# Optimization experiments

Hardware: AMD Instinct MI355X
Metric: run time of the kernel (lower is better)

## Reference

```python
import jax, jax.numpy as jnp
import numpy as np

HIDDEN = 2048
HEADS = 16
HEAD_DIM = HIDDEN // HEADS

def setup_inputs() -> dict:
    key = jax.random.key(0)
    ks = jax.random.split(key, 9)
    B, S = 1, 4096
    scale = 1.0 / np.sqrt(HIDDEN)
    x = jax.random.normal(ks[0], (B, S, HIDDEN), dtype=jnp.float32)
    Wq = jax.random.normal(ks[1], (HIDDEN, HIDDEN), dtype=jnp.float32) * scale
    Wk = jax.random.normal(ks[2], (HIDDEN, HIDDEN), dtype=jnp.float32) * scale
    Wv = jax.random.normal(ks[3], (HIDDEN, HIDDEN), dtype=jnp.float32) * scale
    Wo = jax.random.normal(ks[4], (HIDDEN, HIDDEN), dtype=jnp.float32) * scale
    bq = jax.random.normal(ks[5], (HIDDEN,), dtype=jnp.float32) * 0.01
    bk = jax.random.normal(ks[6], (HIDDEN,), dtype=jnp.float32) * 0.01
    bv = jax.random.normal(ks[7], (HIDDEN,), dtype=jnp.float32) * 0.01
    bo = jax.random.normal(ks[8], (HIDDEN,), dtype=jnp.float32) * 0.01
    return {"x": x, "Wq": Wq, "bq": bq, "Wk": Wk, "bk": bk, "Wv": Wv, "bv": bv, "Wo": Wo, "bo": bo}

def reference(x, Wq, bq, Wk, bk, Wv, bv, Wo, bo):
    B, S, D = x.shape
    H, Hd = HEADS, HEAD_DIM
    # projections (nn.Linear: x @ W^T + b)
    Q = (x @ Wq.T + bq).reshape(B, S, H, Hd).transpose(0, 2, 1, 3)  # [B,H,S,Hd]
    K = (x @ Wk.T + bk).reshape(B, S, H, Hd).transpose(0, 2, 1, 3)
    V = (x @ Wv.T + bv).reshape(B, S, H, Hd).transpose(0, 2, 1, 3)
    scores = jnp.einsum('bhqd,bhkd->bhqk', Q, K) / jnp.sqrt(jnp.float32(Hd))
    attn = jax.nn.softmax(scores, axis=-1)
    out = jnp.einsum('bhqk,bhkd->bhqd', attn, V)  # [B,H,S,Hd]
    out = out.transpose(0, 2, 1, 3).reshape(B, S, D)
    return out @ Wo.T + bo
```

## Files before the change

### kernel.cpp

```cpp
#include <hip/hip_runtime.h>

#define S_LEN  4096
#define DMODEL 2048
#define NHEADS 16
#define HDIM   128

typedef __bf16 bf16x8 __attribute__((ext_vector_type(8)));
typedef __bf16 bf16x2 __attribute__((ext_vector_type(2)));
typedef float  f32x4  __attribute__((ext_vector_type(4)));

__device__ __forceinline__ unsigned short f2b(float f) {
    unsigned int u = __float_as_uint(f);
    unsigned int r = (u + 0x7fffu + ((u >> 16) & 1u)) >> 16;
    return (unsigned short)r;
}

__device__ __forceinline__ unsigned int pkbf16(float a, float b) {
#if __has_builtin(__builtin_amdgcn_cvt_pk_bf16_f32)
    bf16x2 t = __builtin_amdgcn_cvt_pk_bf16_f32(a, b);
    return *(unsigned int*)&t;
#else
    return (unsigned int)f2b(a) | ((unsigned int)f2b(b) << 16);
#endif
}

__device__ __forceinline__ f32x4 mfma16(bf16x8 a, bf16x8 b, f32x4 c) {
    return __builtin_amdgcn_mfma_f32_16x16x32_bf16(a, b, c, 0, 0, 0);
}

__device__ __forceinline__ void ldg2lds16(const void* g, void* l) {
    __builtin_amdgcn_global_load_lds(
        (__attribute__((address_space(1))) void*)(void*)g,
        (__attribute__((address_space(3))) void*)l, 16, 0, 0);
}

__global__ __launch_bounds__(256) void cvt_bf16(
    const float* __restrict__ src, unsigned short* __restrict__ dst, int n4)
{
    int i = blockIdx.x * blockDim.x + threadIdx.x;
    if (i < n4) {
        float4 v = ((const float4*)src)[i];
        uint2 h;
        h.x = pkbf16(v.x, v.y); h.y = pkbf16(v.z, v.w);
        ((uint2*)dst)[i] = h;
    }
}

__global__ __launch_bounds__(256) void cvt_bf16_w4(
    const float* __restrict__ w0, const float* __restrict__ w1,
    const float* __restrict__ w2, const float* __restrict__ w3,
    unsigned short* __restrict__ d0, unsigned short* __restrict__ d1,
    unsigned short* __restrict__ d2, unsigned short* __restrict__ d3)
{
    const int z = blockIdx.y;
    const float* src = (z == 0) ? w0 : (z == 1) ? w1 : (z == 2) ? w2 : w3;
    unsigned short* dst = (z == 0) ? d0 : (z == 1) ? d1 : (z == 2) ? d2 : d3;
    int i = blockIdx.x * blockDim.x + threadIdx.x;
    float4 v = ((const float4*)src)[i];
    uint2 h;
    h.x = pkbf16(v.x, v.y); h.y = pkbf16(v.z, v.w);
    ((uint2*)dst)[i] = h;
}

__global__ __launch_bounds__(256, 2) void gemm_qkv(
    const unsigned short* __restrict__ xb,
    const unsigned short* __restrict__ Wqb, const float* __restrict__ bq,
    const unsigned short* __restrict__ Wkb, const float* __restrict__ bk,
    const unsigned short* __restrict__ Wvb, const float* __restrict__ bv,
    unsigned short* __restrict__ Qb, unsigned short* __restrict__ Kb,
    unsigned short* __restrict__ Vb)
{
    const int z = blockIdx.z;
    const unsigned short* B = (z == 0) ? Wqb : (z == 1) ? Wkb : Wvb;
    const float* bias        = (z == 0) ? bq  : (z == 1) ? bk  : bv;
    unsigned short* C        = (z == 0) ? Qb  : (z == 1) ? Kb  : Vb;
    const float oscale = (z == 0) ? 0.12751743f : 1.0f;

    __shared__ alignas(16) unsigned short As[128 * 32];
    __shared__ alignas(16) unsigned short Bs[128 * 32];

    const int tid = threadIdx.x;
    const int m0 = blockIdx.y * 128, n0 = blockIdx.x * 128;
    const int w = tid >> 6, lane = tid & 63, lo = lane & 15, qd = lane >> 4;
    const int wm = (w >> 1) * 64, wn = (w & 1) * 64;
    const int rsel = lane >> 2, csel = (lane & 3) * 8;

    f32x4 acc[4][4] = {};

    for (int k0 = 0; k0 < DMODEL; k0 += 32) {
#pragma unroll
        for (int i = 0; i < 2; i++) {
            int c = w * 2 + i;
            ldg2lds16(&xb[(size_t)(m0 + c * 16 + rsel) * DMODEL + k0 + csel],
                      &As[c * 512]);
            ldg2lds16(&B [(size_t)(n0 + c * 16 + rsel) * DMODEL + k0 + csel],
                      &Bs[c * 512]);
        }
        __syncthreads();

        bf16x8 af[4], bfr[4];
#pragma unroll
        for (int i = 0; i < 4; i++)
            af[i] = *(const bf16x8*)&As[(wm + i * 16 + lo) * 32 + qd * 8];
#pragma unroll
        for (int j = 0; j < 4; j++)
            bfr[j] = *(const bf16x8*)&Bs[(wn + j * 16 + lo) * 32 + qd * 8];
#pragma unroll
        for (int i = 0; i < 4; i++)
#pragma unroll
            for (int j = 0; j < 4; j++)
                acc[i][j] = mfma16(af[i], bfr[j], acc[i][j]);
        __syncthreads();
    }

#pragma unroll
    for (int j = 0; j < 4; j++) {
        int n = n0 + wn + j * 16 + lo;
        float bv_ = bias[n];
#pragma unroll
        for (int i = 0; i < 4; i++) {
#pragma unroll
            for (int r = 0; r < 4; r++) {
                int m = m0 + wm + i * 16 + qd * 4 + r;
                C[(size_t)m * DMODEL + n] = f2b((acc[i][j][r] + bv_) * oscale);
            }
        }
    }
}

__global__ __launch_bounds__(256, 2) void gemm_out(
    const unsigned short* __restrict__ Aatt, const unsigned short* __restrict__ Wob,
    const float* __restrict__ bo, float* __restrict__ out)
{
    __shared__ alignas(16) unsigned short As[128 * 32];
    __shared__ alignas(16) unsigned short Bs[128 * 32];

    const int tid = threadIdx.x;
    const int m0 = blockIdx.y * 128, n0 = blockIdx.x * 128;
    const int w = tid >> 6, lane = tid & 63, lo = lane & 15, qd = lane >> 4;
    const int wm = (w >> 1) * 64, wn = (w & 1) * 64;
    const int rsel = lane >> 2, csel = (lane & 3) * 8;

    f32x4 acc[4][4] = {};

    for (int k0 = 0; k0 < DMODEL; k0 += 32) {
#pragma unroll
        for (int i = 0; i < 2; i++) {
            int c = w * 2 + i;
            ldg2lds16(&Aatt[(size_t)(m0 + c * 16 + rsel) * DMODEL + k0 + csel],
                      &As[c * 512]);
            ldg2lds16(&Wob [(size_t)(n0 + c * 16 + rsel) * DMODEL + k0 + csel],
                      &Bs[c * 512]);
        }
        __syncthreads();

        bf16x8 af[4], bfr[4];
#pragma unroll
        for (int i = 0; i < 4; i++)
            af[i] = *(const bf16x8*)&As[(wm + i * 16 + lo) * 32 + qd * 8];
#pragma unroll
        for (int j = 0; j < 4; j++)
            bfr[j] = *(const bf16x8*)&Bs[(wn + j * 16 + lo) * 32 + qd * 8];
#pragma unroll
        for (int i = 0; i < 4; i++)
#pragma unroll
            for (int j = 0; j < 4; j++)
                acc[i][j] = mfma16(af[i], bfr[j], acc[i][j]);
        __syncthreads();
    }

#pragma unroll
    for (int j = 0; j < 4; j++) {
        int n = n0 + wn + j * 16 + lo;
        float bv_ = bo[n];
#pragma unroll
        for (int i = 0; i < 4; i++) {
#pragma unroll
            for (int r = 0; r < 4; r++) {
                int m = m0 + wm + i * 16 + qd * 4 + r;
                out[(size_t)m * DMODEL + n] = acc[i][j][r] + bv_;
            }
        }
    }
}

__global__ __launch_bounds__(256) void transpose_v(
    const unsigned short* __restrict__ Vb, unsigned short* __restrict__ Vt)
{
    __shared__ unsigned short tile[64 * 67];
    const int s0 = blockIdx.x * 64;
    const int d0 = blockIdx.y * 64;
    const int tid = threadIdx.x;
#pragma unroll
    for (int i = 0; i < 2; i++) {
        int chunk = tid + i * 256;
        int r = chunk >> 3, c8 = (chunk & 7) * 8;
        uint4 v = *(const uint4*)&Vb[(size_t)(s0 + r) * DMODEL + d0 + c8];
        const unsigned short* p = (const unsigned short*)&v;
#pragma unroll
        for (int j = 0; j < 8; j++) tile[r * 67 + c8 + j] = p[j];
    }
    __syncthreads();
#pragma unroll
    for (int i = 0; i < 2; i++) {
        int chunk = tid + i * 256;
        int r = chunk >> 3, c8 = (chunk & 7) * 8;
        unsigned short tmp[8];
#pragma unroll
        for (int j = 0; j < 8; j++) tmp[j] = tile[(c8 + j) * 67 + r];
        *(uint4*)&Vt[(size_t)(d0 + r) * S_LEN + s0 + c8] = *(uint4*)tmp;
    }
}

__global__ __launch_bounds__(256, 4) void attn_kernel(
    const unsigned short* __restrict__ Qb, const unsigned short* __restrict__ Kb,
    const unsigned short* __restrict__ Vt, unsigned short* __restrict__ Ob)
{
    const int id = blockIdx.x;
    const int xcd = id & 7, slot = id >> 3;
    const int h  = (xcd << 1) | (slot >> 6);
    const int q0 = (slot & 63) * 64;

    __shared__ alignas(16) unsigned short Ks[64 * 128];
    __shared__ alignas(16) unsigned short Vts[128 * 64];
    __shared__ alignas(16) unsigned short Ps[4][16 * 64];

    const int tid = threadIdx.x;
    const int w = tid >> 6, lane = tid & 63, lo = lane & 15, qd = lane >> 4;

    bf16x8 qf[4];
    {
        const unsigned short* qrow =
            &Qb[(size_t)(q0 + w * 16 + lo) * DMODEL + h * HDIM];
#pragma unroll
        for (int kk = 0; kk < 4; kk++)
            qf[kk] = *(const bf16x8*)&qrow[kk * 32 + qd * 8];
    }

    f32x4 o_acc[8] = {};
    float l_run = 0.f;

    for (int kb = 0; kb < S_LEN / 64; kb++) {
        const int key0 = kb * 64;

#pragma unroll
        for (int i = 0; i < 4; i++) {
            int r = w * 16 + i * 4 + (lane >> 4);
            int c = (lane & 15) ^ (r & 7);
            ldg2lds16(&Kb[(size_t)(key0 + r) * DMODEL + h * HDIM + c * 8],
                      &Ks[(w * 16 + i * 4) * 128]);
        }
#pragma unroll
        for (int i = 0; i < 4; i++) {
            int r = w * 32 + i * 8 + (lane >> 3);
            int c = (lane & 7) ^ (r & 7);
            ldg2lds16(&Vt[(size_t)(h * HDIM + r) * S_LEN + key0 + c * 8],
                      &Vts[(w * 32 + i * 8) * 64]);
        }
        __syncthreads();

        f32x4 s[4] = {};
        __builtin_amdgcn_s_setprio(1);
#pragma unroll
        for (int kk = 0; kk < 4; kk++) {
#pragma unroll
            for (int t = 0; t < 4; t++) {
                bf16x8 kf = *(const bf16x8*)
                    &Ks[(t * 16 + lo) * 128 + (((kk * 4 + qd) ^ (lo & 7)) * 8)];
                s[t] = mfma16(kf, qf[kk], s[t]);
            }
        }
        __builtin_amdgcn_s_setprio(0);

        {
            const int row = lo;
            float lsum = 0.f;
#pragma unroll
            for (int t = 0; t < 4; t++) {
                float p0 = __builtin_amdgcn_exp2f(s[t][0]);
                float p1 = __builtin_amdgcn_exp2f(s[t][1]);
                float p2 = __builtin_amdgcn_exp2f(s[t][2]);
                float p3 = __builtin_amdgcn_exp2f(s[t][3]);
                lsum += (p0 + p1) + (p2 + p3);
                uint2 pkv;
                pkv.x = pkbf16(p0, p1);
                pkv.y = pkbf16(p2, p3);
                int swz = (t * 2 + (qd >> 1)) ^ (lo & 7);
                *(uint2*)&Ps[w][row * 64 + swz * 8 + (qd & 1) * 4] = pkv;
            }
            l_run += lsum;
        }
        asm volatile("s_waitcnt lgkmcnt(0)" ::: "memory");

        __builtin_amdgcn_s_setprio(1);
#pragma unroll
        for (int kk = 0; kk < 2; kk++) {
            bf16x8 pf = *(const bf16x8*)
                &Ps[w][lo * 64 + (((kk * 4 + qd) ^ (lo & 7)) * 8)];
#pragma unroll
            for (int dt = 0; dt < 8; dt++) {
                bf16x8 vf = *(const bf16x8*)
                    &Vts[(dt * 16 + lo) * 64 + (((kk * 4 + qd) ^ (lo & 7)) * 8)];
                o_acc[dt] = mfma16(pf, vf, o_acc[dt]);
            }
        }
        __builtin_amdgcn_s_setprio(0);

        __syncthreads();
    }

    {
        float l = l_run;
        l += __shfl_xor(l, 16);
        l += __shfl_xor(l, 32);
        float inv_l[4];
#pragma unroll
        for (int r = 0; r < 4; r++)
            inv_l[r] = 1.0f / __shfl(l, qd * 4 + r);
#pragma unroll
        for (int dt = 0; dt < 8; dt++) {
#pragma unroll
            for (int r = 0; r < 4; r++) {
                int row = q0 + w * 16 + qd * 4 + r;
                int col = h * HDIM + dt * 16 + lo;
                Ob[(size_t)row * DMODEL + col] = f2b(o_acc[dt][r] * inv_l[r]);
            }
        }
    }
}

extern "C" void kernel_launch(void* const* d_in, const int* in_sizes, int n_in,
                              void* d_out, int out_size, void* d_ws, size_t ws_size,
                              hipStream_t stream)
{
    const float* x  = (const float*)d_in[0];
    const float* Wq = (const float*)d_in[1];
    const float* bq = (const float*)d_in[2];
    const float* Wk = (const float*)d_in[3];
    const float* bk = (const float*)d_in[4];
    const float* Wv = (const float*)d_in[5];
    const float* bv = (const float*)d_in[6];
    const float* Wo = (const float*)d_in[7];
    const float* bo = (const float*)d_in[8];
    float* out = (float*)d_out;

    const size_t N = (size_t)S_LEN * DMODEL;
    const size_t W = (size_t)DMODEL * DMODEL;
    unsigned short* Qb  = (unsigned short*)d_ws;
    unsigned short* Kb  = Qb + N;
    unsigned short* Vb  = Kb + N;
    unsigned short* xbv = Vb + N;
    unsigned short* Wqb = xbv + N;
    unsigned short* Wkb = Wqb + W;
    unsigned short* Wvb = Wkb + W;
    unsigned short* Wob = Wvb + W;
    unsigned short* Vt  = xbv;
    unsigned short* Ob  = Vb;

    cvt_bf16<<<(int)(N / 4 / 256), 256, 0, stream>>>(x, xbv, (int)(N / 4));
    cvt_bf16_w4<<<dim3((unsigned)(W / 4 / 256), 4), 256, 0, stream>>>(
        Wq, Wk, Wv, Wo, Wqb, Wkb, Wvb, Wob);

    gemm_qkv<<<dim3(DMODEL / 128, S_LEN / 128, 3), 256, 0, stream>>>(
        xbv, Wqb, bq, Wkb, bk, Wvb, bv, Qb, Kb, Vb);

    transpose_v<<<dim3(S_LEN / 64, DMODEL / 64), 256, 0, stream>>>(Vb, Vt);

    attn_kernel<<<1024, 256, 0, stream>>>(Qb, Kb, Vt, Ob);

    gemm_out<<<dim3(DMODEL / 128, S_LEN / 128), 256, 0, stream>>>(Ob, Wob, bo, out);
}
```

Before: 507.2 us.

## Use 32x32 MFMA in attention with register-resident P and split-K waves

Rewrites the attention inner loop to use 32x32x16 bf16 MFMA. Waves are split into two query halves and two key halves. P is turned into the A operand in registers via permlane32 swaps instead of a round trip through LDS, and the two key-half partial outputs are reduced through shared memory at the end. The aim is fewer LDS reads and writes per block and better MFMA efficiency, at the cost of more registers, so occupancy drops from 4 to 3 blocks per CU, plus an extra final reduction.

```diff
diff --git a/kernel.cpp b/kernel.cpp
--- a/kernel.cpp
+++ b/kernel.cpp
@@ -8,6 +8,7 @@
 typedef __bf16 bf16x8 __attribute__((ext_vector_type(8)));
 typedef __bf16 bf16x2 __attribute__((ext_vector_type(2)));
 typedef float  f32x4  __attribute__((ext_vector_type(4)));
+typedef float  f32x16 __attribute__((ext_vector_type(16)));
 
 __device__ __forceinline__ unsigned short f2b(float f) {
     unsigned int u = __float_as_uint(f);
@@ -26,6 +27,10 @@
 
 __device__ __forceinline__ f32x4 mfma16(bf16x8 a, bf16x8 b, f32x4 c) {
     return __builtin_amdgcn_mfma_f32_16x16x32_bf16(a, b, c, 0, 0, 0);
+}
+
+__device__ __forceinline__ f32x16 mfma32(bf16x8 a, bf16x8 b, f32x16 c) {
+    return __builtin_amdgcn_mfma_f32_32x32x16_bf16(a, b, c, 0, 0, 0);
 }
 
 __device__ __forceinline__ void ldg2lds16(const void* g, void* l) {
@@ -212,7 +217,7 @@
     }
 }
 
-__global__ __launch_bounds__(256, 4) void attn_kernel(
+__global__ __launch_bounds__(256, 3) void attn_kernel(
     const unsigned short* __restrict__ Qb, const unsigned short* __restrict__ Kb,
     const unsigned short* __restrict__ Vt, unsigned short* __restrict__ Ob)
 {
@@ -221,24 +226,31 @@
     const int h  = (xcd << 1) | (slot >> 6);
     const int q0 = (slot & 63) * 64;
 
-    __shared__ alignas(16) unsigned short Ks[64 * 128];
-    __shared__ alignas(16) unsigned short Vts[128 * 64];
-    __shared__ alignas(16) unsigned short Ps[4][16 * 64];
+    __shared__ alignas(16) unsigned char smem[33280];
+    unsigned short* Ks  = (unsigned short*)smem;
+    unsigned short* Vts = (unsigned short*)(smem + 16384);
+    float* Of = (float*)smem;
+    float* Lf = (float*)(smem + 32768);
 
     const int tid = threadIdx.x;
-    const int w = tid >> 6, lane = tid & 63, lo = lane & 15, qd = lane >> 4;
-
-    bf16x8 qf[4];
+    const int w = tid >> 6, lane = tid & 63;
+    const int qw = w >> 1, kw = w & 1;
+    const int l31 = lane & 31, hi = lane >> 5;
+    const int sw7 = l31 & 7;
+
+    bf16x8 qf[8];
     {
         const unsigned short* qrow =
-            &Qb[(size_t)(q0 + w * 16 + lo) * DMODEL + h * HDIM];
-#pragma unroll
-        for (int kk = 0; kk < 4; kk++)
-            qf[kk] = *(const bf16x8*)&qrow[kk * 32 + qd * 8];
-    }
-
-    f32x4 o_acc[8] = {};
+            &Qb[(size_t)(q0 + qw * 32 + l31) * DMODEL + h * HDIM];
+#pragma unroll
+        for (int sl = 0; sl < 8; sl++)
+            qf[sl] = *(const bf16x8*)&qrow[sl * 16 + hi * 8];
+    }
+
+    f32x16 o_acc[4] = {};
     float l_run = 0.f;
+
+    const int krow = kw * 32 + l31;
 
     for (int kb = 0; kb < S_LEN / 64; kb++) {
         const int key0 = kb * 64;
@@ -259,49 +271,49 @@
         }
         __syncthreads();
 
-        f32x4 s[4] = {};
+        f32x16 s = {};
         __builtin_amdgcn_s_setprio(1);
 #pragma unroll
-        for (int kk = 0; kk < 4; kk++) {
-#pragma unroll
-            for (int t = 0; t < 4; t++) {
-                bf16x8 kf = *(const bf16x8*)
-                    &Ks[(t * 16 + lo) * 128 + (((kk * 4 + qd) ^ (lo & 7)) * 8)];
-                s[t] = mfma16(kf, qf[kk], s[t]);
-            }
+        for (int sl = 0; sl < 8; sl++) {
+            bf16x8 kf = *(const bf16x8*)
+                &Ks[krow * 128 + (((2 * sl + hi) ^ sw7) * 8)];
+            s = mfma32(kf, qf[sl], s);
         }
         __builtin_amdgcn_s_setprio(0);
 
+        float p[16];
         {
-            const int row = lo;
-            float lsum = 0.f;
-#pragma unroll
-            for (int t = 0; t < 4; t++) {
-                float p0 = __builtin_amdgcn_exp2f(s[t][0]);
-                float p1 = __builtin_amdgcn_exp2f(s[t][1]);
-                float p2 = __builtin_amdgcn_exp2f(s[t][2]);
-                float p3 = __builtin_amdgcn_exp2f(s[t][3]);
-                lsum += (p0 + p1) + (p2 + p3);
-                uint2 pkv;
-                pkv.x = pkbf16(p0, p1);
-                pkv.y = pkbf16(p2, p3);
-                int swz = (t * 2 + (qd >> 1)) ^ (lo & 7);
-                *(uint2*)&Ps[w][row * 64 + swz * 8 + (qd & 1) * 4] = pkv;
-            }
-            l_run += lsum;
-        }
-        asm volatile("s_waitcnt lgkmcnt(0)" ::: "memory");
+            float ls = 0.f;
+#pragma unroll
+            for (int r = 0; r < 16; r++) {
+                p[r] = __builtin_amdgcn_exp2f(s[r]);
+                ls += p[r];
+            }
+            l_run += ls;
+        }
+
+        bf16x8 pa[2];
+#pragma unroll
+        for (int k2 = 0; k2 < 2; k2++) {
+            unsigned int c0 = pkbf16(p[8 * k2 + 0], p[8 * k2 + 1]);
+            unsigned int c1 = pkbf16(p[8 * k2 + 2], p[8 * k2 + 3]);
+            unsigned int c2 = pkbf16(p[8 * k2 + 4], p[8 * k2 + 5]);
+            unsigned int c3 = pkbf16(p[8 * k2 + 6], p[8 * k2 + 7]);
+            asm("v_permlane32_swap_b32 %0, %1" : "+v"(c0), "+v"(c2));
+            asm("v_permlane32_swap_b32 %0, %1" : "+v"(c1), "+v"(c3));
+            uint4 u; u.x = c0; u.y = c1; u.z = c2; u.w = c3;
+            pa[k2] = *(bf16x8*)&u;
+        }
 
         __builtin_amdgcn_s_setprio(1);
 #pragma unroll
-        for (int kk = 0; kk < 2; kk++) {
-            bf16x8 pf = *(const bf16x8*)
-                &Ps[w][lo * 64 + (((kk * 4 + qd) ^ (lo & 7)) * 8)];
-#pragma unroll
-            for (int dt = 0; dt < 8; dt++) {
+        for (int k2 = 0; k2 < 2; k2++) {
+            const int gch = 4 * kw + 2 * k2 + hi;
+#pragma unroll
+            for (int dt = 0; dt < 4; dt++) {
                 bf16x8 vf = *(const bf16x8*)
-                    &Vts[(dt * 16 + lo) * 64 + (((kk * 4 + qd) ^ (lo & 7)) * 8)];
-                o_acc[dt] = mfma16(pf, vf, o_acc[dt]);
+                    &Vts[(dt * 32 + l31) * 64 + ((gch ^ sw7) * 8)];
+                o_acc[dt] = mfma32(pa[k2], vf, o_acc[dt]);
             }
         }
         __builtin_amdgcn_s_setprio(0);
@@ -309,23 +321,37 @@
         __syncthreads();
     }
 
-    {
-        float l = l_run;
-        l += __shfl_xor(l, 16);
-        l += __shfl_xor(l, 32);
-        float inv_l[4];
-#pragma unroll
-        for (int r = 0; r < 4; r++)
-            inv_l[r] = 1.0f / __shfl(l, qd * 4 + r);
-#pragma unroll
-        for (int dt = 0; dt < 8; dt++) {
-#pragma unroll
-            for (int r = 0; r < 4; r++) {
-                int row = q0 + w * 16 + qd * 4 + r;
-                int col = h * HDIM + dt * 16 + lo;
-                Ob[(size_t)row * DMODEL + col] = f2b(o_acc[dt][r] * inv_l[r]);
-            }
-        }
+    float l = l_run + __shfl_xor(l_run, 32);
+
+    if (kw == 1) {
+#pragma unroll
+        for (int dt = 0; dt < 4; dt++)
+#pragma unroll
+            for (int r = 0; r < 16; r++) {
+                int row = (r & 3) + 8 * (r >> 2) + 4 * hi;
+                Of[(qw * 32 + row) * 128 + dt * 32 + l31] = o_acc[dt][r];
+            }
+    }
+    if (hi == 0) Lf[(qw * 2 + kw) * 32 + l31] = l;
+    __syncthreads();
+
+    if (kw == 0) {
+        float linv[16];
+#pragma unroll
+        for (int r = 0; r < 16; r++) {
+            int row = (r & 3) + 8 * (r >> 2) + 4 * hi;
+            linv[r] = 1.0f / (Lf[(qw * 2 + 0) * 32 + row] +
+                              Lf[(qw * 2 + 1) * 32 + row]);
+        }
+#pragma unroll
+        for (int dt = 0; dt < 4; dt++)
+#pragma unroll
+            for (int r = 0; r < 16; r++) {
+                int row = (r & 3) + 8 * (r >> 2) + 4 * hi;
+                float v = o_acc[dt][r] + Of[(qw * 32 + row) * 128 + dt * 32 + l31];
+                Ob[(size_t)(q0 + qw * 32 + row) * DMODEL + h * HDIM + dt * 32 + l31]
+                    = f2b(v * linv[r]);
+            }
     }
 }
 
```

New measurement: 525.0 us. 1.04x slower.
